# Kernel optimization log

Measured on AMD Instinct MI355X. Metric: run time of the kernel, lower is better.

Reference implementation:

```python
import jax, jax.numpy as jnp
import numpy as np

N_GRID = 65160   # 181*360 lat-lon grid nodes (= self.size)
N_MESH = 40962   # level-6 icosphere nodes
N_TOT = N_GRID + N_MESH
E = 521280
IN_CH = 96
HID = 256
OUT_CH = 96


def setup_inputs() -> dict:
    key = jax.random.key(0)
    ks = jax.random.split(key, 12)
    inp = {
        'x': jax.random.normal(ks[0], (1, IN_CH, N_MESH), jnp.float32),
        'x_res_grid': jax.random.normal(ks[1], (1, IN_CH, N_GRID), jnp.float32),
        'edge_index': jax.random.randint(ks[2], (2, E), 0, N_TOT, jnp.int64),
        # GCNConv 1 (in_ch -> 256), glorot-ish scale
        'W1': jax.random.normal(ks[3], (IN_CH, HID), jnp.float32) * (2.0 / (IN_CH + HID)) ** 0.5,
        'b1': jnp.zeros((HID,), jnp.float32),
        # GCNConv 2 (256 -> 256)
        'W2': jax.random.normal(ks[4], (HID, HID), jnp.float32) * (2.0 / (HID + HID)) ** 0.5,
        'b2': jnp.zeros((HID,), jnp.float32),
        # Lmodel2: Linear(256,256) -> Linear(256,out_ch), xavier_normal
        'Wl1': jax.random.normal(ks[5], (HID, HID), jnp.float32) * (2.0 / (HID + HID)) ** 0.5,
        'bl1': jnp.zeros((HID,), jnp.float32),
        'Wl2': jax.random.normal(ks[6], (HID, OUT_CH), jnp.float32) * (2.0 / (HID + OUT_CH)) ** 0.5,
        'bl2': jnp.zeros((OUT_CH,), jnp.float32),
    }
    return inp


def _gcn_norm(edge_index, n_nodes):
    # PyG gcn_norm with add_self_loops=True, edge_weight=1
    loop = jnp.arange(n_nodes, dtype=edge_index.dtype)
    src = jnp.concatenate([edge_index[0], loop])
    dst = jnp.concatenate([edge_index[1], loop])
    deg = jnp.zeros((n_nodes,), jnp.float32).at[dst].add(1.0)
    dinv = jnp.where(deg > 0, jax.lax.rsqrt(deg), 0.0)
    norm = dinv[src] * dinv[dst]  # [E+N]
    return src, dst, norm


def _gcn_conv(h, W, b, src, dst, norm):
    # h: [B, N, C] -> [B, N, H]; x' = D^-1/2 (A+I) D^-1/2 (h W) + b
    m = h @ W                                   # [B, N, H]
    msg = m[:, src, :] * norm[None, :, None]    # [B, E+N, H]
    agg = jnp.zeros(m.shape, m.dtype).at[:, dst].add(msg)
    return agg + b


def reference(x, x_res_grid, edge_index, W1, b1, W2, b2, Wl1, bl1, Wl2, bl2):
    nodes = jnp.concatenate([x_res_grid, x], axis=-1)  # [B, C, N]
    h = nodes.transpose(0, 2, 1)                       # [B, N, C]
    n = h.shape[1]
    src, dst, norm = _gcn_norm(edge_index, n)
    h = _gcn_conv(h, W1, b1, src, dst, norm)
    h = jax.nn.gelu(h, approximate=False)              # torch nn.GELU (exact erf)
    h = _gcn_conv(h, W2, b2, src, dst, norm)           # [B, N, 256]
    g = h[:, :N_GRID, :]                               # slice grid nodes
    out = (g @ Wl1 + bl1) @ Wl2 + bl2                  # [B, size, out_ch]
    return out.transpose(0, 2, 1)                      # [B, out_ch, size]
```

## Files before the change

kernel.cpp:

```cpp
#include <hip/hip_runtime.h>
#include <math.h>

#define N_GRID 65160
#define N_MESH 40962
#define N_TOT  106122
#define NE     521280
#define IN_CH  96
#define HID    256
#define OUT_CH 96

typedef __attribute__((ext_vector_type(8))) short bf16x8;
typedef __attribute__((ext_vector_type(4))) float f32x4;

__device__ __forceinline__ unsigned short f2bf(float f) {
  unsigned u = __float_as_uint(f);
  return (unsigned short)((u + 0x7FFFu + ((u >> 16) & 1u)) >> 16);
}
__device__ __forceinline__ float bf2f(unsigned short s) {
  return __uint_as_float(((unsigned)s) << 16);
}
__device__ __forceinline__ void unp8(uint4 v, float* f) {
  f[0] = __uint_as_float(v.x << 16); f[1] = __uint_as_float(v.x & 0xFFFF0000u);
  f[2] = __uint_as_float(v.y << 16); f[3] = __uint_as_float(v.y & 0xFFFF0000u);
  f[4] = __uint_as_float(v.z << 16); f[5] = __uint_as_float(v.z & 0xFFFF0000u);
  f[6] = __uint_as_float(v.w << 16); f[7] = __uint_as_float(v.w & 0xFFFF0000u);
}

__global__ void k_concat_transpose(const float* __restrict__ xg, const float* __restrict__ xm,
                                   unsigned short* __restrict__ h) {
  __shared__ float tile[IN_CH][65];
  int base = blockIdx.x * 64;
  int t = threadIdx.x;
#pragma unroll
  for (int it = 0; it < 24; ++it) {
    int lin = t + it * 256;
    int c  = lin >> 6;
    int n0 = lin & 63;
    int n = base + n0;
    float v = 0.f;
    if (n < N_TOT) {
      v = (n < N_GRID) ? xg[(size_t)c * N_GRID + n]
                       : xm[(size_t)c * N_MESH + (n - N_GRID)];
    }
    tile[c][n0] = v;
  }
  __syncthreads();
#pragma unroll
  for (int it = 0; it < 24; ++it) {
    int lin = t + it * 256;
    int c  = lin % 96;
    int n0 = lin / 96;
    int n = base + n0;
    if (n < N_TOT) h[(size_t)n * IN_CH + c] = f2bf(tile[c][n0]);
  }
}

__global__ void k_transpose_out(const float* __restrict__ tb, float* __restrict__ out) {
  __shared__ float tile[IN_CH][65];
  int base = blockIdx.x * 64;
  int t = threadIdx.x;
#pragma unroll
  for (int it = 0; it < 24; ++it) {
    int lin = t + it * 256;
    int c  = lin % 96;
    int n0 = lin / 96;
    int n = base + n0;
    if (n < N_GRID) tile[c][n0] = tb[(size_t)n * 96 + c];
  }
  __syncthreads();
#pragma unroll
  for (int it = 0; it < 24; ++it) {
    int lin = t + it * 256;
    int c  = lin >> 6;
    int n0 = lin & 63;
    int n = base + n0;
    if (n < N_GRID) out[(size_t)c * N_GRID + n] = tile[c][n0];
  }
}

__global__ void k_zeroi(int* __restrict__ p, int n) {
  int i = blockIdx.x * 256 + threadIdx.x;
  if (i < n) p[i] = 0;
}

__global__ void k_hist(const int* __restrict__ dst, int* __restrict__ deg) {
  int e = blockIdx.x * 256 + threadIdx.x;
  if (e < NE) atomicAdd(&deg[dst[e]], 1);
}

__global__ void k_blocksum(const int* __restrict__ deg, int* __restrict__ bsum, int n) {
  __shared__ int s[256];
  int i = blockIdx.x * 256 + threadIdx.x;
  s[threadIdx.x] = (i < n) ? deg[i] : 0;
  __syncthreads();
  for (int st = 128; st > 0; st >>= 1) {
    if (threadIdx.x < st) s[threadIdx.x] += s[threadIdx.x + st];
    __syncthreads();
  }
  if (threadIdx.x == 0) bsum[blockIdx.x] = s[0];
}

__global__ void k_scanbsum(int* __restrict__ bsum, int nb) {
  __shared__ int s[512];
  int t = threadIdx.x;
  int v = (t < nb) ? bsum[t] : 0;
  s[t] = v;
  __syncthreads();
  for (int off = 1; off < 512; off <<= 1) {
    int x = (t >= off) ? s[t - off] : 0;
    __syncthreads();
    s[t] += x;
    __syncthreads();
  }
  if (t < nb) bsum[t] = s[t] - v;
}

__global__ void k_offsets(const int* __restrict__ deg, const int* __restrict__ bsum,
                          int* __restrict__ off, int* __restrict__ cur,
                          float* __restrict__ dinv, int n) {
  __shared__ int s[256];
  int i = blockIdx.x * 256 + threadIdx.x;
  int v = (i < n) ? deg[i] : 0;
  s[threadIdx.x] = v;
  __syncthreads();
  for (int o = 1; o < 256; o <<= 1) {
    int x = (threadIdx.x >= o) ? s[threadIdx.x - o] : 0;
    __syncthreads();
    s[threadIdx.x] += x;
    __syncthreads();
  }
  if (i < n) {
    int e = bsum[blockIdx.x] + s[threadIdx.x] - v;
    off[i] = e;
    cur[i] = e;
    dinv[i] = rsqrtf(1.0f + (float)v);
  }
  if (i == 0) off[n] = NE;
}

__global__ void k_fillcsr(const int* __restrict__ src, const int* __restrict__ dst,
                          int* __restrict__ cur, int* __restrict__ csrc) {
  int e = blockIdx.x * 256 + threadIdx.x;
  if (e < NE) {
    int p = atomicAdd(&cur[dst[e]], 1);
    csrc[p] = src[e];
  }
}

__global__ void k_gather96(const int* __restrict__ off, const int* __restrict__ csrc,
                           const float* __restrict__ dinv, const unsigned short* __restrict__ h,
                           unsigned short* __restrict__ agg) {
  int i = blockIdx.x * 256 + threadIdx.x;
  if (i >= N_TOT * 12) return;
  int n = i / 12;
  int c8 = (i % 12) << 3;
  float di = dinv[n];
  float acc[8], f[8];
  uint4 v = *(const uint4*)(h + (size_t)n * 96 + c8);
  unp8(v, f);
  float w0 = di * di;
#pragma unroll
  for (int j = 0; j < 8; ++j) acc[j] = f[j] * w0;
  int e0 = off[n], e1 = off[n + 1];
  int e = e0;
  for (; e + 3 < e1; e += 4) {
    int s0 = csrc[e], s1 = csrc[e + 1], s2 = csrc[e + 2], s3 = csrc[e + 3];
    float wa = dinv[s0] * di, wb = dinv[s1] * di, wc = dinv[s2] * di, wd = dinv[s3] * di;
    uint4 u0 = *(const uint4*)(h + (size_t)s0 * 96 + c8);
    uint4 u1 = *(const uint4*)(h + (size_t)s1 * 96 + c8);
    uint4 u2 = *(const uint4*)(h + (size_t)s2 * 96 + c8);
    uint4 u3 = *(const uint4*)(h + (size_t)s3 * 96 + c8);
    float g0[8], g1[8], g2[8], g3[8];
    unp8(u0, g0); unp8(u1, g1); unp8(u2, g2); unp8(u3, g3);
#pragma unroll
    for (int j = 0; j < 8; ++j) acc[j] += g0[j] * wa + g1[j] * wb + g2[j] * wc + g3[j] * wd;
  }
  for (; e < e1; ++e) {
    int s = csrc[e];
    float w = dinv[s] * di;
    uint4 u = *(const uint4*)(h + (size_t)s * 96 + c8);
    unp8(u, f);
#pragma unroll
    for (int j = 0; j < 8; ++j) acc[j] += f[j] * w;
  }
  uint4 o;
  o.x = (unsigned)f2bf(acc[0]) | ((unsigned)f2bf(acc[1]) << 16);
  o.y = (unsigned)f2bf(acc[2]) | ((unsigned)f2bf(acc[3]) << 16);
  o.z = (unsigned)f2bf(acc[4]) | ((unsigned)f2bf(acc[5]) << 16);
  o.w = (unsigned)f2bf(acc[6]) | ((unsigned)f2bf(acc[7]) << 16);
  *(uint4*)(agg + (size_t)n * 96 + c8) = o;
}

__global__ void k_gather96p(const int* __restrict__ off, const int* __restrict__ csrc,
                            const float* __restrict__ dinv, const unsigned short* __restrict__ p,
                            const float* __restrict__ bc, float* __restrict__ tb) {
  int i = blockIdx.x * 256 + threadIdx.x;
  if (i >= N_GRID * 12) return;
  int n = i / 12;
  int c8 = (i % 12) << 3;
  float di = dinv[n];
  float acc[8], f[8];
  uint4 v = *(const uint4*)(p + (size_t)n * 96 + c8);
  unp8(v, f);
  float w0 = di * di;
#pragma unroll
  for (int j = 0; j < 8; ++j) acc[j] = f[j] * w0;
  int e0 = off[n], e1 = off[n + 1];
  int e = e0;
  for (; e + 3 < e1; e += 4) {
    int s0 = csrc[e], s1 = csrc[e + 1], s2 = csrc[e + 2], s3 = csrc[e + 3];
    float wa = dinv[s0] * di, wb = dinv[s1] * di, wc = dinv[s2] * di, wd = dinv[s3] * di;
    uint4 u0 = *(const uint4*)(p + (size_t)s0 * 96 + c8);
    uint4 u1 = *(const uint4*)(p + (size_t)s1 * 96 + c8);
    uint4 u2 = *(const uint4*)(p + (size_t)s2 * 96 + c8);
    uint4 u3 = *(const uint4*)(p + (size_t)s3 * 96 + c8);
    float g0[8], g1[8], g2[8], g3[8];
    unp8(u0, g0); unp8(u1, g1); unp8(u2, g2); unp8(u3, g3);
#pragma unroll
    for (int j = 0; j < 8; ++j) acc[j] += g0[j] * wa + g1[j] * wb + g2[j] * wc + g3[j] * wd;
  }
  for (; e < e1; ++e) {
    int s = csrc[e];
    float w = dinv[s] * di;
    uint4 u = *(const uint4*)(p + (size_t)s * 96 + c8);
    unp8(u, f);
#pragma unroll
    for (int j = 0; j < 8; ++j) acc[j] += f[j] * w;
  }
  float* row = tb + (size_t)n * 96 + c8;
  *(float4*)(row)     = make_float4(acc[0] + bc[c8 + 0], acc[1] + bc[c8 + 1],
                                    acc[2] + bc[c8 + 2], acc[3] + bc[c8 + 3]);
  *(float4*)(row + 4) = make_float4(acc[4] + bc[c8 + 4], acc[5] + bc[c8 + 5],
                                    acc[6] + bc[c8 + 6], acc[7] + bc[c8 + 7]);
}

__global__ __launch_bounds__(256, 2) void k_wgemm96(const float* __restrict__ A, const float* __restrict__ bvec,
                                                    const float* __restrict__ B, float* __restrict__ C,
                                                    int M, int K) {
  __shared__ float As[64][33];
  __shared__ float Bs[64][100];
  int t = threadIdx.x;
  int tx = t & 15, ty = t >> 4;
  int bm = blockIdx.x * 32;
  float acc[2][6] = {};
  for (int kc = 0; kc < K; kc += 64) {
#pragma unroll
    for (int it = 0; it < 2; ++it) {
      int idx = t + it * 256;
      int r = idx >> 4, k4 = (idx & 15) << 2;
      int gr = bm + r;
      float4 v = make_float4(0.f, 0.f, 0.f, 0.f);
      if (gr < M) {
        const float* src = (gr < M - 1) ? (A + (size_t)gr * K + kc + k4) : (bvec + kc + k4);
        v = *(const float4*)src;
      }
      As[k4 + 0][r] = v.x;
      As[k4 + 1][r] = v.y;
      As[k4 + 2][r] = v.z;
      As[k4 + 3][r] = v.w;
    }
#pragma unroll
    for (int it = 0; it < 6; ++it) {
      int idx = t + it * 256;
      int k = idx / 24, j4 = (idx % 24) << 2;
      float4 v = *(const float4*)(B + (size_t)(kc + k) * 96 + j4);
      *(float4*)&Bs[k][j4] = v;
    }
    __syncthreads();
#pragma unroll
    for (int k = 0; k < 64; ++k) {
      float a0 = As[k][ty * 2], a1 = As[k][ty * 2 + 1];
      float w[6];
      *(float2*)&w[0] = *(const float2*)&Bs[k][tx * 6];
      *(float2*)&w[2] = *(const float2*)&Bs[k][tx * 6 + 2];
      *(float2*)&w[4] = *(const float2*)&Bs[k][tx * 6 + 4];
#pragma unroll
      for (int j = 0; j < 6; ++j) { acc[0][j] += a0 * w[j]; acc[1][j] += a1 * w[j]; }
    }
    __syncthreads();
  }
#pragma unroll
  for (int i = 0; i < 2; ++i) {
    int gr = bm + ty * 2 + i;
    if (gr >= M) continue;
    float* row = C + (size_t)gr * 96 + tx * 6;
    row[0] = acc[i][0]; row[1] = acc[i][1]; row[2] = acc[i][2];
    row[3] = acc[i][3]; row[4] = acc[i][4]; row[5] = acc[i][5];
  }
}

__global__ void k_bc_final(const float* __restrict__ r1, const float* __restrict__ r2,
                           const float* __restrict__ bl2, float* __restrict__ bc) {
  int j = threadIdx.x;
  if (j < OUT_CH) bc[j] = r1[j] + r2[j] + bl2[j];
}

__global__ void k_cast_w1t(const float* __restrict__ W1, unsigned short* __restrict__ W1bt) {
  int idx = blockIdx.x * 256 + threadIdx.x;
  if (idx >= 256 * 96) return;
  int n = idx / 96, k = idx % 96;
  W1bt[idx] = f2bf(W1[(size_t)k * 256 + n]);
}
__global__ void k_cast_wct(const float* __restrict__ Wc, unsigned short* __restrict__ Wcbt) {
  int idx = blockIdx.x * 256 + threadIdx.x;
  if (idx >= 96 * 256) return;
  int n = idx / 256, k = idx % 256;
  Wcbt[idx] = f2bf(Wc[(size_t)k * 96 + n]);
}

#define SWZ(row, g) (((row) << 7) + (((g) ^ ((row) & 7)) << 3))
#define SWZH(row, g) (((row) << 8) + (((g) ^ ((row) & 7)) << 3))
__global__ __launch_bounds__(256, 3) void k_mlp(const unsigned short* __restrict__ A,
                                                const unsigned short* __restrict__ W1bt,
                                                const float* __restrict__ bias1,
                                                const unsigned short* __restrict__ Wcbt,
                                                unsigned short* __restrict__ P, int M) {
  __shared__ unsigned short Hs[64 * 256];
  __shared__ unsigned short Ws[64 * 128];
  int t = threadIdx.x;
  int wave = t >> 6, lane = t & 63;
  int l15 = lane & 15, lhi = lane >> 4;
  int bm = blockIdx.x * 64;

  int arowl = wave * 16 + l15;
  bool aok = (bm + arowl) < M;
  const unsigned short* ap = A + (size_t)(bm + arowl) * 96 + lhi * 8;
  bf16x8 a0 = aok ? *(const bf16x8*)(ap)      : (bf16x8){0,0,0,0,0,0,0,0};
  bf16x8 a1 = aok ? *(const bf16x8*)(ap + 32) : (bf16x8){0,0,0,0,0,0,0,0};
  bf16x8 a2 = aok ? *(const bf16x8*)(ap + 64) : (bf16x8){0,0,0,0,0,0,0,0};
  int hrow = wave * 16 + lhi * 4;

  for (int c = 0; c < 4; ++c) {
    __syncthreads();
#pragma unroll
    for (int it = 0; it < 3; ++it) {
      int idx = t + it * 256;
      int row = idx / 12, g = idx % 12;
      *(uint4*)&Ws[SWZ(row, g)] = *(const uint4*)(W1bt + (size_t)(c * 64 + row) * 96 + g * 8);
    }
    __syncthreads();
#pragma unroll
    for (int fl = 0; fl < 4; ++fl) {
      int f = c * 4 + fl;
      int wrow = fl * 16 + l15;
      bf16x8 w0_ = *(const bf16x8*)&Ws[SWZ(wrow, 0 + lhi)];
      bf16x8 w1_ = *(const bf16x8*)&Ws[SWZ(wrow, 4 + lhi)];
      bf16x8 w2_ = *(const bf16x8*)&Ws[SWZ(wrow, 8 + lhi)];
      f32x4 acc = (f32x4){0.f, 0.f, 0.f, 0.f};
      acc = __builtin_amdgcn_mfma_f32_16x16x32_bf16(a0, w0_, acc, 0, 0, 0);
      acc = __builtin_amdgcn_mfma_f32_16x16x32_bf16(a1, w1_, acc, 0, 0, 0);
      acc = __builtin_amdgcn_mfma_f32_16x16x32_bf16(a2, w2_, acc, 0, 0, 0);
      int col = f * 16 + l15;
      float bv = bias1[col];
#pragma unroll
      for (int r = 0; r < 4; ++r) {
        float x = acc[r] + bv;
        x = 0.5f * x * (1.0f + erff(x * 0.70710678118654752f));
        int row = hrow + r;
        Hs[SWZH(row, col >> 3) + (col & 7)] = f2bf(x);
      }
    }
  }

  int orow = wave * 16 + lhi * 4;
  for (int tf = 0; tf < 2; ++tf) {
    f32x4 accC[3];
#pragma unroll
    for (int fl = 0; fl < 3; ++fl) accC[fl] = (f32x4){0.f, 0.f, 0.f, 0.f};
    for (int kh = 0; kh < 2; ++kh) {
      __syncthreads();
#pragma unroll
      for (int it = 0; it < 3; ++it) {
        int idx = t + it * 256;
        int row = idx >> 4, g = idx & 15;
        *(uint4*)&Ws[SWZ(row, g)] =
            *(const uint4*)(Wcbt + (size_t)(tf * 48 + row) * 256 + kh * 128 + g * 8);
      }
      __syncthreads();
#pragma unroll
      for (int fl = 0; fl < 3; ++fl) {
        int wrow = fl * 16 + l15;
        int harow = wave * 16 + l15;
#pragma unroll
        for (int ks = 0; ks < 4; ++ks) {
          bf16x8 av = *(const bf16x8*)&Hs[SWZH(harow, (kh * 4 + ks) * 4 + lhi)];
          bf16x8 wv = *(const bf16x8*)&Ws[SWZ(wrow, ks * 4 + lhi)];
          accC[fl] = __builtin_amdgcn_mfma_f32_16x16x32_bf16(av, wv, accC[fl], 0, 0, 0);
        }
      }
    }
#pragma unroll
    for (int fl = 0; fl < 3; ++fl) {
      int col = (tf * 3 + fl) * 16 + l15;
#pragma unroll
      for (int r = 0; r < 4; ++r) {
        int row = bm + orow + r;
        if (row < M) P[(size_t)row * 96 + col] = f2bf(accC[fl][r]);
      }
    }
  }
}

extern "C" void kernel_launch(void* const* d_in, const int* in_sizes, int n_in,
                              void* d_out, int out_size, void* d_ws, size_t ws_size,
                              hipStream_t stream) {
  const float* xm  = (const float*)d_in[0];
  const float* xg  = (const float*)d_in[1];
  const int*   ei  = (const int*)d_in[2];
  const float* W1  = (const float*)d_in[3];
  const float* b1  = (const float*)d_in[4];
  const float* W2  = (const float*)d_in[5];
  const float* b2  = (const float*)d_in[6];
  const float* Wl1 = (const float*)d_in[7];
  const float* bl1 = (const float*)d_in[8];
  const float* Wl2 = (const float*)d_in[9];
  const float* bl2 = (const float*)d_in[10];
  float* out = (float*)d_out;

  float* W0 = (float*)d_ws;
  const size_t MB = (size_t)N_GRID * 256;
  int*   deg  = (int*)(W0 + MB);
  int*   off  = deg + N_TOT;
  int*   cur  = off + N_TOT + 1;
  int*   bsum = cur + N_TOT;
  int*   csrc = bsum + 512;
  float* dinv = (float*)(csrc + NE);
  size_t p1off = ((size_t)(dinv + N_TOT - W0) + 3) & ~(size_t)3;
  float* P1 = W0 + p1off;
  float* P2 = P1 + 257 * 96;
  float* bc = P2 + 257 * 96;
  size_t wboff = ((size_t)(bc + 96 - W0) + 3) & ~(size_t)3;
  unsigned short* W1bt = (unsigned short*)(W0 + wboff);
  unsigned short* Wcbt = W1bt + 256 * 96;
  size_t RH = (wboff + 24576 + 3) & ~(size_t)3;
  unsigned short* hb = (unsigned short*)(W0 + RH);
  unsigned short* agg1b = (unsigned short*)W0;
  unsigned short* p = (unsigned short*)(hb + (size_t)N_TOT * 96 + 16);
  p = (unsigned short*)(((size_t)p + 15) & ~(size_t)15);
  float* tb = W0 + (size_t)6 * 1024 * 1024;

  const int* esrc = ei;
  const int* edst = ei + NE;
  dim3 b256(256);
  const int NB_N = (N_TOT + 255) / 256;

  k_concat_transpose<<<dim3((N_TOT + 63) / 64), b256, 0, stream>>>(xg, xm, hb);

  k_zeroi<<<dim3(NB_N), b256, 0, stream>>>(deg, N_TOT);
  k_hist<<<dim3((NE + 255) / 256), b256, 0, stream>>>(edst, deg);
  k_blocksum<<<dim3(NB_N), b256, 0, stream>>>(deg, bsum, N_TOT);
  k_scanbsum<<<dim3(1), dim3(512), 0, stream>>>(bsum, NB_N);
  k_offsets<<<dim3(NB_N), b256, 0, stream>>>(deg, bsum, off, cur, dinv, N_TOT);
  k_fillcsr<<<dim3((NE + 255) / 256), b256, 0, stream>>>(esrc, edst, cur, csrc);
  k_cast_w1t<<<dim3(96), b256, 0, stream>>>(W1, W1bt);
  k_wgemm96<<<dim3(9), b256, 0, stream>>>(Wl1, bl1, Wl2, P1, 257, HID);
  k_wgemm96<<<dim3(9), b256, 0, stream>>>(W2, b2, P1, P2, 257, HID);
  k_bc_final<<<dim3(1), dim3(96), 0, stream>>>(P1 + 256 * 96, P2 + 256 * 96, bl2, bc);
  k_cast_wct<<<dim3(96), b256, 0, stream>>>(P2, Wcbt);

  k_gather96<<<dim3((N_TOT * 12 + 255) / 256), b256, 0, stream>>>(off, csrc, dinv, hb, agg1b);

  k_mlp<<<dim3((N_TOT + 63) / 64), b256, 0, stream>>>(agg1b, W1bt, b1, Wcbt, p, N_TOT);

  k_gather96p<<<dim3((N_GRID * 12 + 255) / 256), b256, 0, stream>>>(off, csrc, dinv, p, bc, tb);

  k_transpose_out<<<dim3((N_GRID + 63) / 64), b256, 0, stream>>>(tb, out);
}
```

Measured before the change: 229.3 us.

## Split hidden dimension in k_mlp to halve LDS and raise occupancy; fuse bias kernel

The fused MLP kernel now processes the 256-wide hidden activation in two 128-column halves. Each half is computed, stored to LDS and immediately consumed by the second GEMM, which accumulates into six persistent accumulators. This halves the shared-memory tile and raises the launch bound from 3 to 4 blocks per CU to improve occupancy. Separately, the tiny bias-combine kernel is folded into the weight-cast kernel to remove one launch. The trade-off is more live accumulator registers and extra synchronisation rounds per block.

```diff
diff --git a/kernel.cpp b/kernel.cpp
--- a/kernel.cpp
+++ b/kernel.cpp
@@ -289,33 +289,30 @@
   }
 }
 
-__global__ void k_bc_final(const float* __restrict__ r1, const float* __restrict__ r2,
-                           const float* __restrict__ bl2, float* __restrict__ bc) {
-  int j = threadIdx.x;
-  if (j < OUT_CH) bc[j] = r1[j] + r2[j] + bl2[j];
-}
-
 __global__ void k_cast_w1t(const float* __restrict__ W1, unsigned short* __restrict__ W1bt) {
   int idx = blockIdx.x * 256 + threadIdx.x;
   if (idx >= 256 * 96) return;
   int n = idx / 96, k = idx % 96;
   W1bt[idx] = f2bf(W1[(size_t)k * 256 + n]);
 }
-__global__ void k_cast_wct(const float* __restrict__ Wc, unsigned short* __restrict__ Wcbt) {
+__global__ void k_cast_wct(const float* __restrict__ P2, const float* __restrict__ r1,
+                           const float* __restrict__ bl2, unsigned short* __restrict__ Wcbt,
+                           float* __restrict__ bc) {
   int idx = blockIdx.x * 256 + threadIdx.x;
+  if (blockIdx.x == 0 && threadIdx.x < OUT_CH)
+    bc[threadIdx.x] = r1[threadIdx.x] + P2[256 * 96 + threadIdx.x] + bl2[threadIdx.x];
   if (idx >= 96 * 256) return;
   int n = idx / 256, k = idx % 256;
-  Wcbt[idx] = f2bf(Wc[(size_t)k * 96 + n]);
+  Wcbt[idx] = f2bf(P2[(size_t)k * 96 + n]);
 }
 
 #define SWZ(row, g) (((row) << 7) + (((g) ^ ((row) & 7)) << 3))
-#define SWZH(row, g) (((row) << 8) + (((g) ^ ((row) & 7)) << 3))
-__global__ __launch_bounds__(256, 3) void k_mlp(const unsigned short* __restrict__ A,
+__global__ __launch_bounds__(256, 4) void k_mlp(const unsigned short* __restrict__ A,
                                                 const unsigned short* __restrict__ W1bt,
                                                 const float* __restrict__ bias1,
                                                 const unsigned short* __restrict__ Wcbt,
                                                 unsigned short* __restrict__ P, int M) {
-  __shared__ unsigned short Hs[64 * 256];
+  __shared__ unsigned short Hs[64 * 128];
   __shared__ unsigned short Ws[64 * 128];
   int t = threadIdx.x;
   int wave = t >> 6, lane = t & 63;
@@ -329,52 +326,55 @@
   bf16x8 a1 = aok ? *(const bf16x8*)(ap + 32) : (bf16x8){0,0,0,0,0,0,0,0};
   bf16x8 a2 = aok ? *(const bf16x8*)(ap + 64) : (bf16x8){0,0,0,0,0,0,0,0};
   int hrow = wave * 16 + lhi * 4;
-
-  for (int c = 0; c < 4; ++c) {
-    __syncthreads();
-#pragma unroll
-    for (int it = 0; it < 3; ++it) {
-      int idx = t + it * 256;
-      int row = idx / 12, g = idx % 12;
-      *(uint4*)&Ws[SWZ(row, g)] = *(const uint4*)(W1bt + (size_t)(c * 64 + row) * 96 + g * 8);
-    }
-    __syncthreads();
-#pragma unroll
-    for (int fl = 0; fl < 4; ++fl) {
-      int f = c * 4 + fl;
-      int wrow = fl * 16 + l15;
-      bf16x8 w0_ = *(const bf16x8*)&Ws[SWZ(wrow, 0 + lhi)];
-      bf16x8 w1_ = *(const bf16x8*)&Ws[SWZ(wrow, 4 + lhi)];
-      bf16x8 w2_ = *(const bf16x8*)&Ws[SWZ(wrow, 8 + lhi)];
-      f32x4 acc = (f32x4){0.f, 0.f, 0.f, 0.f};
-      acc = __builtin_amdgcn_mfma_f32_16x16x32_bf16(a0, w0_, acc, 0, 0, 0);
-      acc = __builtin_amdgcn_mfma_f32_16x16x32_bf16(a1, w1_, acc, 0, 0, 0);
-      acc = __builtin_amdgcn_mfma_f32_16x16x32_bf16(a2, w2_, acc, 0, 0, 0);
-      int col = f * 16 + l15;
-      float bv = bias1[col];
-#pragma unroll
-      for (int r = 0; r < 4; ++r) {
-        float x = acc[r] + bv;
-        x = 0.5f * x * (1.0f + erff(x * 0.70710678118654752f));
-        int row = hrow + r;
-        Hs[SWZH(row, col >> 3) + (col & 7)] = f2bf(x);
+  int orow = wave * 16 + lhi * 4;
+
+  f32x4 accC[6];
+#pragma unroll
+  for (int q = 0; q < 6; ++q) accC[q] = (f32x4){0.f, 0.f, 0.f, 0.f};
+
+  for (int hf = 0; hf < 2; ++hf) {
+    for (int c = 0; c < 2; ++c) {
+      __syncthreads();
+#pragma unroll
+      for (int it = 0; it < 3; ++it) {
+        int idx = t + it * 256;
+        int row = idx / 12, g = idx % 12;
+        *(uint4*)&Ws[SWZ(row, g)] =
+            *(const uint4*)(W1bt + (size_t)(hf * 128 + c * 64 + row) * 96 + g * 8);
       }
-    }
-  }
-
-  int orow = wave * 16 + lhi * 4;
-  for (int tf = 0; tf < 2; ++tf) {
-    f32x4 accC[3];
-#pragma unroll
-    for (int fl = 0; fl < 3; ++fl) accC[fl] = (f32x4){0.f, 0.f, 0.f, 0.f};
-    for (int kh = 0; kh < 2; ++kh) {
+      __syncthreads();
+#pragma unroll
+      for (int fl = 0; fl < 4; ++fl) {
+        int floc = c * 4 + fl;
+        int wrow = fl * 16 + l15;
+        bf16x8 w0_ = *(const bf16x8*)&Ws[SWZ(wrow, 0 + lhi)];
+        bf16x8 w1_ = *(const bf16x8*)&Ws[SWZ(wrow, 4 + lhi)];
+        bf16x8 w2_ = *(const bf16x8*)&Ws[SWZ(wrow, 8 + lhi)];
+        f32x4 acc = (f32x4){0.f, 0.f, 0.f, 0.f};
+        acc = __builtin_amdgcn_mfma_f32_16x16x32_bf16(a0, w0_, acc, 0, 0, 0);
+        acc = __builtin_amdgcn_mfma_f32_16x16x32_bf16(a1, w1_, acc, 0, 0, 0);
+        acc = __builtin_amdgcn_mfma_f32_16x16x32_bf16(a2, w2_, acc, 0, 0, 0);
+        int col = (hf * 8 + floc) * 16 + l15;
+        int colh = floc * 16 + l15;
+        float bv = bias1[col];
+#pragma unroll
+        for (int r = 0; r < 4; ++r) {
+          float x = acc[r] + bv;
+          x = 0.5f * x * (1.0f + erff(x * 0.70710678118654752f));
+          int row = hrow + r;
+          Hs[SWZ(row, colh >> 3) + (colh & 7)] = f2bf(x);
+        }
+      }
+    }
+
+    for (int tf = 0; tf < 2; ++tf) {
       __syncthreads();
 #pragma unroll
       for (int it = 0; it < 3; ++it) {
         int idx = t + it * 256;
         int row = idx >> 4, g = idx & 15;
         *(uint4*)&Ws[SWZ(row, g)] =
-            *(const uint4*)(Wcbt + (size_t)(tf * 48 + row) * 256 + kh * 128 + g * 8);
+            *(const uint4*)(Wcbt + (size_t)(tf * 48 + row) * 256 + hf * 128 + g * 8);
       }
       __syncthreads();
 #pragma unroll
@@ -383,20 +383,21 @@
         int harow = wave * 16 + l15;
 #pragma unroll
         for (int ks = 0; ks < 4; ++ks) {
-          bf16x8 av = *(const bf16x8*)&Hs[SWZH(harow, (kh * 4 + ks) * 4 + lhi)];
+          bf16x8 av = *(const bf16x8*)&Hs[SWZ(harow, ks * 4 + lhi)];
           bf16x8 wv = *(const bf16x8*)&Ws[SWZ(wrow, ks * 4 + lhi)];
-          accC[fl] = __builtin_amdgcn_mfma_f32_16x16x32_bf16(av, wv, accC[fl], 0, 0, 0);
+          accC[tf * 3 + fl] = __builtin_amdgcn_mfma_f32_16x16x32_bf16(av, wv, accC[tf * 3 + fl], 0, 0, 0);
         }
       }
     }
-#pragma unroll
-    for (int fl = 0; fl < 3; ++fl) {
-      int col = (tf * 3 + fl) * 16 + l15;
-#pragma unroll
-      for (int r = 0; r < 4; ++r) {
-        int row = bm + orow + r;
-        if (row < M) P[(size_t)row * 96 + col] = f2bf(accC[fl][r]);
-      }
+  }
+
+#pragma unroll
+  for (int q = 0; q < 6; ++q) {
+    int col = (q / 3) * 48 + (q % 3) * 16 + l15;
+#pragma unroll
+    for (int r = 0; r < 4; ++r) {
+      int row = bm + orow + r;
+      if (row < M) P[(size_t)row * 96 + col] = f2bf(accC[q][r]);
     }
   }
 }
@@ -455,8 +456,7 @@
   k_cast_w1t<<<dim3(96), b256, 0, stream>>>(W1, W1bt);
   k_wgemm96<<<dim3(9), b256, 0, stream>>>(Wl1, bl1, Wl2, P1, 257, HID);
   k_wgemm96<<<dim3(9), b256, 0, stream>>>(W2, b2, P1, P2, 257, HID);
-  k_bc_final<<<dim3(1), dim3(96), 0, stream>>>(P1 + 256 * 96, P2 + 256 * 96, bl2, bc);
-  k_cast_wct<<<dim3(96), b256, 0, stream>>>(P2, Wcbt);
+  k_cast_wct<<<dim3(96), b256, 0, stream>>>(P2, P1 + 256 * 96, bl2, Wcbt, bc);
 
   k_gather96<<<dim3((N_TOT * 12 + 255) / 256), b256, 0, stream>>>(off, csrc, dinv, hb, agg1b);
 
```

After: 222.8 us. 2.8% less time.
